# Kernel tuning notes

Hardware: AMD Instinct MI355X
Metric: run time of the kernel (lower is better)

## Reference

```python
import jax, jax.numpy as jnp
import numpy as np

B, T, D_IN = 64, 365, 10
D_MODEL, N_HEAD, D_K = 256, 16, 8
D_HEAD = D_MODEL // N_HEAD  # 16, value head dim
MAX_POS = 365 + 2 * 30      # max_position + 2*max_temporal_shift = 425
BN_EPS = 1e-5


def _pos_table(n_pos, d, temp=1000.0):
    # standard sinusoidal table (frozen in the original via Embedding.from_pretrained)
    pos = np.arange(n_pos)[:, None].astype(np.float64)
    i = np.arange(d)[None, :]
    angle = pos / np.power(temp, 2 * (i // 2) / d)
    tab = np.where(i % 2 == 0, np.sin(angle), np.cos(angle))
    return jnp.asarray(tab, jnp.float32)

POS_TABLE = _pos_table(MAX_POS, D_MODEL)


def _linear_layer(x, W, b, g, beta):
    # LinearLayer = Linear -> BatchNorm1d (train-mode batch stats, per-feature) -> ReLU
    y = x @ W.T + b
    ax = tuple(range(y.ndim - 1))
    mu = y.mean(ax, keepdims=True)
    var = y.var(ax, keepdims=True)  # biased var, matches torch BN
    y = (y - mu) * jax.lax.rsqrt(var + BN_EPS) * g + beta
    return jax.nn.relu(y)


def _forward(positions, x, w1, b1, g1, e1, w2, b2, g2, e2, w3, b3, g3, e3,
             ws1, ws2, wi, bi, gi, ei, wk, bk, wq, bq, wm, bm, gm, em,
             wd1, bd1, gd1, ed1, wd2, bd2, gd2, ed2, wc, bc):
    # channel MLP encoder: 10 -> 64 -> 128 -> 256
    out = _linear_layer(x, w1, b1, g1, e1)
    out = _linear_layer(out, w2, b2, g2, e2)
    out = _linear_layer(out, w3, b3, g3, e3)                    # [B,T,256]
    # channel SE attention: avgpool over time, 2 linears (no bias), sigmoid, residual
    pooled = out.mean(axis=1, keepdims=True)                     # [B,1,256]
    att = jax.nn.sigmoid(jax.nn.relu(pooled @ ws1.T) @ ws2.T)    # [B,1,256]
    out = att * pooled + out                                     # broadcast residual
    # temporal attention block
    h = _linear_layer(out, wi, bi, gi, ei)                       # inconv -> [B,T,256]
    e = h + POS_TABLE[positions]                                 # add positional encoding
    q = (e @ wq.T + bq).reshape(B, T, N_HEAD, D_K)
    k = (e @ wk.T + bk).reshape(B, T, N_HEAD, D_K)
    v = e.reshape(B, T, N_HEAD, D_HEAD)
    # 'cross' attention: full score matrix, mean over key dim, softmax over query dim
    scores = jnp.einsum('bthd,bshd->bhts', q, k) / jnp.sqrt(jnp.float32(D_K))  # [B,H,T,T]
    scores = scores.mean(axis=-1)                                # [B,H,T]
    a = jax.nn.softmax(scores, axis=-1)                          # [B,H,T]
    y = jnp.einsum('bht,bthe->bhe', a, v).reshape(B, D_MODEL)    # [B,256]
    y = _linear_layer(y, wm, bm, gm, em)                         # mlp 256 -> 128
    # decoder: 128 -> 64 -> 32 -> num_classes
    z = _linear_layer(y, wd1, bd1, gd1, ed1)
    z = _linear_layer(z, wd2, bd2, gd2, ed2)
    return z @ wc.T + bc                                         # logits [B,10]


def setup_inputs():
    key = jax.random.key(0)
    ks = jax.random.split(key, 16)
    n = lambda i, sh: jax.random.normal(ks[i], sh, jnp.float32) * 0.05
    z, o = jnp.zeros, jnp.ones
    return {
        'x': jax.random.normal(ks[0], (B, T, D_IN), jnp.float32),
        'positions': jnp.sort(jax.random.randint(ks[1], (B, T), 0, MAX_POS), axis=-1),
        'w1': n(2, (64, D_IN)), 'b1': z(64), 'g1': o(64), 'e1': z(64),
        'w2': n(3, (128, 64)), 'b2': z(128), 'g2': o(128), 'e2': z(128),
        'w3': n(4, (256, 128)), 'b3': z(256), 'g3': o(256), 'e3': z(256),
        'ws1': n(5, (16, 256)), 'ws2': n(6, (256, 16)),
        'wi': n(7, (256, 256)), 'bi': z(256), 'gi': o(256), 'ei': z(256),
        'wk': n(8, (128, 256)), 'bk': z(128),
        'wq': n(9, (128, 256)), 'bq': z(128),
        'wm': n(10, (128, 256)), 'bm': z(128), 'gm': o(128), 'em': z(128),
        'wd1': n(11, (64, 128)), 'bd1': z(64), 'gd1': o(64), 'ed1': z(64),
        'wd2': n(12, (32, 64)), 'bd2': z(32), 'gd2': o(32), 'ed2': z(32),
        'wc': n(13, (10, 32)), 'bc': z(10),
    }


def reference(x, positions, w1, b1, g1, e1, w2, b2, g2, e2, w3, b3, g3, e3,
              ws1, ws2, wi, bi, gi, ei, wk, bk, wq, bq, wm, bm, gm, em,
              wd1, bd1, gd1, ed1, wd2, bd2, gd2, ed2, wc, bc):
    return _forward(positions, x, w1, b1, g1, e1, w2, b2, g2, e2, w3, b3, g3, e3,
                    ws1, ws2, wi, bi, gi, ei, wk, bk, wq, bq, wm, bm, gm, em,
                    wd1, bd1, gd1, ed1, wd2, bd2, gd2, ed2, wc, bc)
```

## Files before the change

### kernel.cpp

```cpp
#include <hip/hip_runtime.h>
#include <hip/hip_bf16.h>
#include <math.h>

#define TT 365
#define BT 23360
#define NPOS 425

typedef __hip_bfloat16 bf16;
typedef __attribute__((ext_vector_type(8))) short s16x8;
typedef __attribute__((ext_vector_type(4))) float f32x4;

__device__ __forceinline__ float b2f(bf16 v) { return __bfloat162float(v); }
__device__ __forceinline__ bf16  f2b(float v) { return __float2bfloat16(v); }
__device__ __forceinline__ float u2f(unsigned u) { return __uint_as_float(u); }
__device__ __forceinline__ short f2bs(float v) { bf16 h = __float2bfloat16(v); return *reinterpret_cast<short*>(&h); }
__device__ __forceinline__ void unpack8(uint4 raw, float* v) {
    v[0] = u2f(raw.x << 16); v[1] = u2f(raw.x & 0xffff0000u);
    v[2] = u2f(raw.y << 16); v[3] = u2f(raw.y & 0xffff0000u);
    v[4] = u2f(raw.z << 16); v[5] = u2f(raw.z & 0xffff0000u);
    v[6] = u2f(raw.w << 16); v[7] = u2f(raw.w & 0xffff0000u);
}

__global__ __launch_bounds__(256) void prep_kernel(
    float* __restrict__ stats, float* __restrict__ pooled, float* __restrict__ esum,
    const float* __restrict__ w2, const float* __restrict__ w3, const float* __restrict__ wi,
    const float* __restrict__ wq,
    bf16* __restrict__ whi, bf16* __restrict__ wlo, float* __restrict__ tab)
{
    int i = blockIdx.x * 256 + threadIdx.x;
    if (i < 2048)  { stats[i] = 0.f; return; }  i -= 2048;
    if (i < 16384) { pooled[i] = 0.f; return; } i -= 16384;
    if (i < 16384) { esum[i] = 0.f; return; }   i -= 16384;
    if (i < 139264) {
        float w;
        if      (i < 8192)   w = w2[i];
        else if (i < 40960)  w = w3[i - 8192];
        else if (i < 106496) w = wi[i - 40960];
        else                 w = wq[i - 106496];
        bf16 h = f2b(w);
        whi[i] = h;
        wlo[i] = f2b(w - b2f(h));
        return;
    } i -= 139264;
    if (i < 108800) {
        int c = i & 255, p = i >> 8;
        float e = (float)(2 * (c >> 1)) * (1.f / 256.f);
        float ang = (float)p * exp2f(-e * 9.96578428466209f);
        tab[i] = (c & 1) ? cosf(ang) : sinf(ang);
    }
}

__global__ __launch_bounds__(256) void gemm_l1_kernel(
    const float* __restrict__ x,
    const float* __restrict__ W, const float* __restrict__ bias,
    bf16* __restrict__ Y, float* __restrict__ stats)
{
    const int t  = threadIdx.x;
    const int tx = t & 15, ty = t >> 4;
    const int row0 = blockIdx.x * 64;
    __shared__ float As[64][17];
    __shared__ float Ws[16][65];
    __shared__ float red_s[4][64];
    __shared__ float red_q[4][64];
    float acc[4][4];
#pragma unroll
    for (int rr = 0; rr < 4; ++rr)
#pragma unroll
        for (int cc = 0; cc < 4; ++cc) acc[rr][cc] = 0.f;
#pragma unroll
    for (int i = 0; i < 4; ++i) {
        int idx = t + i * 256, r = idx >> 4, c = idx & 15;
        As[r][c] = (c < 10) ? x[(size_t)(row0 + r) * 10 + c] : 0.f;
    }
#pragma unroll
    for (int i = 0; i < 4; ++i) {
        int idx = t + i * 256, c = idx >> 4, kk = idx & 15;
        Ws[kk][c] = (kk < 10) ? W[(size_t)c * 10 + kk] : 0.f;
    }
    __syncthreads();
#pragma unroll
    for (int kk = 0; kk < 10; ++kk) {
        float a[4];
#pragma unroll
        for (int rr = 0; rr < 4; ++rr) a[rr] = As[ty * 4 + rr][kk];
#pragma unroll
        for (int cc = 0; cc < 4; ++cc) {
            float w = Ws[kk][cc * 16 + tx];
#pragma unroll
            for (int rr = 0; rr < 4; ++rr) acc[rr][cc] = fmaf(a[rr], w, acc[rr][cc]);
        }
    }
    float s_cc[4], q_cc[4];
#pragma unroll
    for (int cc = 0; cc < 4; ++cc) { s_cc[cc] = 0.f; q_cc[cc] = 0.f; }
#pragma unroll
    for (int rr = 0; rr < 4; ++rr) {
        int row = row0 + ty * 4 + rr;
#pragma unroll
        for (int cc = 0; cc < 4; ++cc) {
            int col = cc * 16 + tx;
            float v = acc[rr][cc] + bias[col];
            Y[(size_t)row * 64 + col] = f2b(v);
            s_cc[cc] += v; q_cc[cc] += v * v;
        }
    }
    int w = t >> 6;
#pragma unroll
    for (int cc = 0; cc < 4; ++cc) {
        float s = s_cc[cc], q = q_cc[cc];
        s += __shfl_xor(s, 16); q += __shfl_xor(q, 16);
        s += __shfl_xor(s, 32); q += __shfl_xor(q, 32);
        if ((t & 63) < 16) { red_s[w][cc * 16 + tx] = s; red_q[w][cc * 16 + tx] = q; }
    }
    __syncthreads();
    if (t < 64) {
        float s = red_s[0][t] + red_s[1][t] + red_s[2][t] + red_s[3][t];
        float q = red_q[0][t] + red_q[1][t] + red_q[2][t] + red_q[3][t];
        atomicAdd(&stats[t], s);
        atomicAdd(&stats[256 + t], q);
    }
}

template<int MODE, int K>
__global__ __launch_bounds__(256) void mfma_gemm(
    const bf16* __restrict__ A,
    const bf16* __restrict__ Whi, const bf16* __restrict__ Wlo,
    const float* __restrict__ bias,
    bf16* __restrict__ Y, int ldY, float* __restrict__ stats,
    const float* __restrict__ bnstats, const float* __restrict__ bng,
    const float* __restrict__ bnb, const float* __restrict__ sebuf)
{
    constexpr int KC = (K > 128) ? 128 : K;
    __shared__ s16x8 Wl[2][KC / 8][64];
    __shared__ float red_s[4][64];
    __shared__ float red_q[4][64];
    __shared__ float scb[MODE ? K : 1];
    __shared__ float shb[MODE ? K : 1];
    const int t = threadIdx.x, wave = t >> 6, lane = t & 63;
    const int n16 = lane & 15, quad = lane >> 4;
    const int m0 = blockIdx.x * 64 + wave * 16;
    const int col0 = blockIdx.y * 64;
    const int sc_ = t & 63, skg0 = t >> 6;
    const bf16* gh = Whi + (size_t)(col0 + sc_) * K;
    const bf16* gl = Wlo + (size_t)(col0 + sc_) * K;
#pragma unroll
    for (int kg = skg0; kg < KC / 8; kg += 4) {
        Wl[0][kg][sc_] = *(const s16x8*)(gh + kg * 8);
        Wl[1][kg][sc_] = *(const s16x8*)(gl + kg * 8);
    }
    if (MODE) {
        if (t < K) {
            float mu = bnstats[t] * (1.f / (float)BT);
            float var = bnstats[256 + t] * (1.f / (float)BT) - mu * mu;
            float sc = rsqrtf(var + 1e-5f) * bng[t];
            scb[t] = sc; shb[t] = bnb[t] - mu * sc;
        }
    }
    __syncthreads();
    const int arow = m0 + n16;
    const float* sev = (MODE == 2) ? (sebuf + (arow / TT) * 256) : nullptr;
    const bf16* Ap = A + (size_t)arow * K + quad * 8;
    s16x8 af[K / 32];
#pragma unroll
    for (int i = 0; i < K / 32; ++i) {
        s16x8 raw = *(const s16x8*)(Ap + i * 32);
        if (MODE) {
            int kb = i * 32 + quad * 8;
#pragma unroll
            for (int j = 0; j < 8; ++j) {
                float y = u2f(((unsigned)(unsigned short)raw[j]) << 16);
                float v = fmaxf(fmaf(y, scb[kb + j], shb[kb + j]), 0.f);
                if (MODE == 2) v += sev[kb + j];
                raw[j] = f2bs(v);
            }
        }
        af[i] = raw;
    }
    f32x4 acc[4];
    f32x4 zero = {0.f, 0.f, 0.f, 0.f};
#pragma unroll
    for (int ct = 0; ct < 4; ++ct) acc[ct] = zero;
#pragma unroll
    for (int kc = 0; kc < K; kc += KC) {
        if (kc) {
            __syncthreads();
#pragma unroll
            for (int kg = skg0; kg < KC / 8; kg += 4) {
                Wl[0][kg][sc_] = *(const s16x8*)(gh + kc + kg * 8);
                Wl[1][kg][sc_] = *(const s16x8*)(gl + kc + kg * 8);
            }
            __syncthreads();
        }
#pragma unroll
        for (int i = 0; i < KC / 32; ++i) {
            const int kgq = i * 4 + quad;
            const s16x8 a = af[(kc >> 5) + i];
#pragma unroll
            for (int ct = 0; ct < 4; ++ct) {
                s16x8 bl = Wl[1][kgq][ct * 16 + n16];
                s16x8 bh = Wl[0][kgq][ct * 16 + n16];
                acc[ct] = __builtin_amdgcn_mfma_f32_16x16x32_bf16(a, bl, acc[ct], 0, 0, 0);
                acc[ct] = __builtin_amdgcn_mfma_f32_16x16x32_bf16(a, bh, acc[ct], 0, 0, 0);
            }
        }
    }
#pragma unroll
    for (int ct = 0; ct < 4; ++ct) {
        int col = col0 + ct * 16 + n16;
        float bv = bias[col];
        float s = 0.f, q = 0.f;
#pragma unroll
        for (int r = 0; r < 4; ++r) {
            float v = acc[ct][r] + bv;
            int row = m0 + quad * 4 + r;
            Y[(size_t)row * ldY + col] = f2b(v);
            s += v; q += v * v;
        }
        s += __shfl_xor(s, 16); q += __shfl_xor(q, 16);
        s += __shfl_xor(s, 32); q += __shfl_xor(q, 32);
        if (quad == 0) { red_s[wave][ct * 16 + n16] = s; red_q[wave][ct * 16 + n16] = q; }
    }
    if (stats) {
        __syncthreads();
        if (t < 64) {
            float s = red_s[0][t] + red_s[1][t] + red_s[2][t] + red_s[3][t];
            float q = red_q[0][t] + red_q[1][t] + red_q[2][t] + red_q[3][t];
            atomicAdd(&stats[col0 + t], s);
            atomicAdd(&stats[256 + col0 + t], q);
        }
    }
}

__global__ __launch_bounds__(256) void pool_partial_kernel(
    const bf16* __restrict__ Y3, const float* __restrict__ stats,
    const float* __restrict__ g3, const float* __restrict__ e3,
    float* __restrict__ pooled)
{
    const int b = blockIdx.x, part = blockIdx.y, t = threadIdx.x;
    const int cg = t & 31, rs = t >> 5;
    __shared__ float scb[256], shb[256];
    __shared__ float pp[8][256];
    {
        float mu = stats[t] * (1.f / (float)BT);
        float var = stats[256 + t] * (1.f / (float)BT) - mu * mu;
        float sc = rsqrtf(var + 1e-5f) * g3[t];
        scb[t] = sc; shb[t] = e3[t] - mu * sc;
    }
    __syncthreads();
    float acc[8] = {0.f,0.f,0.f,0.f,0.f,0.f,0.f,0.f};
    const int r0 = part * 46;
#pragma unroll
    for (int i = 0; i < 6; ++i) {
        int l = rs + i * 8;
        int r = r0 + l;
        if (l < 46 && r < TT) {
            uint4 raw = *(const uint4*)(Y3 + ((size_t)b * TT + r) * 256 + cg * 8);
            float v[8];
            unpack8(raw, v);
#pragma unroll
            for (int j = 0; j < 8; ++j)
                acc[j] += fmaxf(fmaf(v[j], scb[cg * 8 + j], shb[cg * 8 + j]), 0.f);
        }
    }
#pragma unroll
    for (int j = 0; j < 8; ++j) pp[rs][cg * 8 + j] = acc[j];
    __syncthreads();
    float s = 0.f;
#pragma unroll
    for (int r = 0; r < 8; ++r) s += pp[r][t];
    atomicAdd(&pooled[b * 256 + t], s);
}

__global__ __launch_bounds__(256) void esum_kernel(const bf16* __restrict__ e,
                                                   float* __restrict__ esum)
{
    const int b = blockIdx.x, part = blockIdx.y, t = threadIdx.x;
    const int cg = t & 31, rs = t >> 5;
    __shared__ float pp[8][256];
    float acc[8] = {0.f,0.f,0.f,0.f,0.f,0.f,0.f,0.f};
    const int r0 = part * 46;
#pragma unroll
    for (int i = 0; i < 6; ++i) {
        int l = rs + i * 8;
        int r = r0 + l;
        if (l < 46 && r < TT) {
            uint4 raw = *(const uint4*)(e + ((size_t)b * TT + r) * 256 + cg * 8);
            float v[8];
            unpack8(raw, v);
#pragma unroll
            for (int j = 0; j < 8; ++j) acc[j] += v[j];
        }
    }
#pragma unroll
    for (int j = 0; j < 8; ++j) pp[rs][cg * 8 + j] = acc[j];
    __syncthreads();
    float s = 0.f;
#pragma unroll
    for (int r = 0; r < 8; ++r) s += pp[r][t];
    atomicAdd(&esum[b * 256 + t], s);
}

__global__ __launch_bounds__(256) void se_mlp_kernel(const float* __restrict__ pooled,
                                                     const float* __restrict__ ws1,
                                                     const float* __restrict__ ws2,
                                                     float* __restrict__ se) {
    int b = blockIdx.x, f = threadIdx.x;
    __shared__ float pl[256];
    __shared__ float hidden[16];
    float p = pooled[b * 256 + f] * (1.f / (float)TT);
    pl[f] = p;
    __syncthreads();
    if (f < 16) {
        float h = 0.f;
        for (int k2 = 0; k2 < 256; ++k2) h = fmaf(pl[k2], ws1[f * 256 + k2], h);
        hidden[f] = fmaxf(h, 0.f);
    }
    __syncthreads();
    float a = 0.f;
    for (int k2 = 0; k2 < 16; ++k2) a = fmaf(hidden[k2], ws2[f * 16 + k2], a);
    a = 1.f / (1.f + expf(-a));
    se[b * 256 + f] = a * p;
}

__global__ __launch_bounds__(256) void bnrelu8_kernel(
    const bf16* __restrict__ Y, const float* __restrict__ stats,
    const float* __restrict__ g, const float* __restrict__ beta,
    bf16* __restrict__ Out, const float* __restrict__ tab, const int* __restrict__ pos) {
    int i = (blockIdx.x * 256 + threadIdx.x) * 8;
    int col = i & 255, row = i >> 8;
    uint4 raw = *(const uint4*)(Y + i);
    float v[8];
    unpack8(raw, v);
    const float invM = 1.f / (float)BT;
    const float* tr = tab + pos[row] * 256 + col;
    bf16 tmp[8] __attribute__((aligned(16)));
#pragma unroll
    for (int j = 0; j < 8; ++j) {
        float mu  = stats[col + j] * invM;
        float var = stats[256 + col + j] * invM - mu * mu;
        float o = (v[j] - mu) * rsqrtf(var + 1e-5f) * g[col + j] + beta[col + j];
        tmp[j] = f2b(fmaxf(o, 0.f) + tr[j]);
    }
    *(uint4*)(Out + i) = *(const uint4*)tmp;
}

__global__ __launch_bounds__(64) void attn_kernel(
    const bf16* __restrict__ q, const bf16* __restrict__ e,
    const float* __restrict__ esum, const float* __restrict__ wk,
    const float* __restrict__ bk, float* __restrict__ yv)
{
    __shared__ float aw[368];
    const int b = blockIdx.x, h = blockIdx.y;
    const int lane = threadIdx.x;
    float4 es = *(const float4*)(esum + b * 256 + lane * 4);
    float ks[8];
#pragma unroll
    for (int d = 0; d < 8; ++d) {
        float4 wv = *(const float4*)(wk + (size_t)(h * 8 + d) * 256 + lane * 4);
        ks[d] = es.x * wv.x + es.y * wv.y + es.z * wv.z + es.w * wv.w;
    }
#pragma unroll
    for (int off = 1; off < 64; off <<= 1)
#pragma unroll
        for (int d = 0; d < 8; ++d) ks[d] += __shfl_xor(ks[d], off);
#pragma unroll
    for (int d = 0; d < 8; ++d) ks[d] += (float)TT * bk[h * 8 + d];
    const float scale = 1.f / (sqrtf(8.f) * (float)TT);
    const bf16* qb = q + (size_t)b * TT * 128 + h * 8;
    float sv[6];
    float m = -1e30f;
#pragma unroll
    for (int i = 0; i < 6; ++i) {
        int r = lane + i * 64;
        float s = -1e30f;
        if (r < TT) {
            uint4 raw = *(const uint4*)(qb + (size_t)r * 128);
            float v[8];
            unpack8(raw, v);
            float dot = 0.f;
#pragma unroll
            for (int j = 0; j < 8; ++j) dot = fmaf(v[j], ks[j], dot);
            s = dot * scale;
        }
        sv[i] = s;
        m = fmaxf(m, s);
    }
#pragma unroll
    for (int off = 1; off < 64; off <<= 1) m = fmaxf(m, __shfl_xor(m, off));
    float sum = 0.f;
#pragma unroll
    for (int i = 0; i < 6; ++i) {
        float ev = (sv[i] > -1e29f) ? expf(sv[i] - m) : 0.f;
        sv[i] = ev; sum += ev;
    }
#pragma unroll
    for (int off = 1; off < 64; off <<= 1) sum += __shfl_xor(sum, off);
    float inv = 1.f / sum;
#pragma unroll
    for (int i = 0; i < 6; ++i) {
        int r = lane + i * 64;
        if (r < TT) aw[r] = sv[i] * inv;
    }
    __syncthreads();
    const int half = lane & 1, rs = lane >> 1;
    float acc[8] = {0.f,0.f,0.f,0.f,0.f,0.f,0.f,0.f};
    const bf16* ebase = e + (size_t)b * TT * 256 + h * 16 + half * 8;
#pragma unroll
    for (int i = 0; i < 12; ++i) {
        int r = rs + i * 32;
        if (r < TT) {
            uint4 raw = *(const uint4*)(ebase + (size_t)r * 256);
            float v[8];
            unpack8(raw, v);
            float a = aw[r];
#pragma unroll
            for (int j = 0; j < 8; ++j) acc[j] = fmaf(a, v[j], acc[j]);
        }
    }
#pragma unroll
    for (int off = 2; off < 64; off <<= 1)
#pragma unroll
        for (int j = 0; j < 8; ++j) acc[j] += __shfl_xor(acc[j], off);
    if (lane < 2) {
        float* op = yv + b * 256 + h * 16 + half * 8;
#pragma unroll
        for (int j = 0; j < 8; ++j) op[j] = acc[j];
    }
}

__global__ __launch_bounds__(1024) void tail_kernel(
    const float* __restrict__ yv,
    const float* wm, const float* bm, const float* gm, const float* em,
    const float* wd1, const float* bd1, const float* gd1, const float* ed1,
    const float* wd2, const float* bd2, const float* gd2, const float* ed2,
    const float* wc, const float* bc, float* __restrict__ out)
{
    __shared__ float lds[12352];
    const int t = threadIdx.x;
    const int r = t & 63, cg = t >> 6;
    float* Xq  = lds;
    float* Wp  = lds + 4160;
    float* Z1t = lds;
    float* Wd1h = lds + 8192;
    float* Z2t = lds;
    float* Wd2 = lds + 4096;
    float* Z3t = lds + 6144;
    float* WcL = lds + 8192;

    float acc1[8] = {0.f,0.f,0.f,0.f,0.f,0.f,0.f,0.f};
    const int c01 = cg * 8;
    for (int p = 0; p < 4; ++p) {
        __syncthreads();
        for (int i = t; i < 4096; i += 1024) {
            int kk = i & 63, rr = i >> 6;
            Xq[kk * 65 + rr] = yv[rr * 256 + p * 64 + kk];
        }
        {
            const float4* wm4 = (const float4*)wm;
            float4* Wp4 = (float4*)Wp;
            for (int i = t; i < 2048; i += 1024) {
                int kk4 = i & 15, c = i >> 4;
                Wp4[c * 16 + kk4] = wm4[c * 64 + p * 16 + kk4];
            }
        }
        __syncthreads();
#pragma unroll 4
        for (int k4 = 0; k4 < 16; ++k4) {
            float xv[4];
#pragma unroll
            for (int j = 0; j < 4; ++j) xv[j] = Xq[(k4 * 4 + j) * 65 + r];
#pragma unroll
            for (int c = 0; c < 8; ++c) {
                float4 w = *(const float4*)(Wp + (c01 + c) * 64 + k4 * 4);
                acc1[c] = fmaf(xv[0], w.x, acc1[c]);
                acc1[c] = fmaf(xv[1], w.y, acc1[c]);
                acc1[c] = fmaf(xv[2], w.z, acc1[c]);
                acc1[c] = fmaf(xv[3], w.w, acc1[c]);
            }
        }
    }
    float z1v[8];
#pragma unroll
    for (int c = 0; c < 8; ++c) {
        float v = acc1[c] + bm[c01 + c];
        float s = v, q = v * v;
#pragma unroll
        for (int off = 1; off < 64; off <<= 1) { s += __shfl_xor(s, off); q += __shfl_xor(q, off); }
        float mu = s * (1.f / 64.f), var = q * (1.f / 64.f) - mu * mu;
        z1v[c] = fmaxf((v - mu) * rsqrtf(var + 1e-5f) * gm[c01 + c] + em[c01 + c], 0.f);
    }
    __syncthreads();
#pragma unroll
    for (int c = 0; c < 8; ++c) Z1t[(c01 + c) * 64 + r] = z1v[c];
    float acc2[4] = {0.f, 0.f, 0.f, 0.f};
    const int c02 = cg * 4;
    for (int ph = 0; ph < 2; ++ph) {
        __syncthreads();
        {
            const float4* s4 = (const float4*)wd1;
            float4* d4 = (float4*)Wd1h;
            int kk4 = t & 15, c = t >> 4;
            d4[c * 16 + kk4] = s4[c * 32 + ph * 16 + kk4];
        }
        __syncthreads();
#pragma unroll 4
        for (int k4 = 0; k4 < 16; ++k4) {
            float xv[4];
#pragma unroll
            for (int j = 0; j < 4; ++j) xv[j] = Z1t[(ph * 64 + k4 * 4 + j) * 64 + r];
#pragma unroll
            for (int c = 0; c < 4; ++c) {
                float4 w = *(const float4*)(Wd1h + (c02 + c) * 64 + k4 * 4);
                acc2[c] = fmaf(xv[0], w.x, acc2[c]);
                acc2[c] = fmaf(xv[1], w.y, acc2[c]);
                acc2[c] = fmaf(xv[2], w.z, acc2[c]);
                acc2[c] = fmaf(xv[3], w.w, acc2[c]);
            }
        }
    }
    float z2v[4];
#pragma unroll
    for (int c = 0; c < 4; ++c) {
        float v = acc2[c] + bd1[c02 + c];
        float s = v, q = v * v;
#pragma unroll
        for (int off = 1; off < 64; off <<= 1) { s += __shfl_xor(s, off); q += __shfl_xor(q, off); }
        float mu = s * (1.f / 64.f), var = q * (1.f / 64.f) - mu * mu;
        z2v[c] = fmaxf((v - mu) * rsqrtf(var + 1e-5f) * gd1[c02 + c] + ed1[c02 + c], 0.f);
    }
    __syncthreads();
#pragma unroll
    for (int c = 0; c < 4; ++c) Z2t[(c02 + c) * 64 + r] = z2v[c];
    {
        const float4* s4 = (const float4*)wd2;
        float4* d4 = (float4*)Wd2;
        if (t < 512) d4[t] = s4[t];
    }
    __syncthreads();
    float acc3[2] = {0.f, 0.f};
    const int c03 = cg * 2;
#pragma unroll 4
    for (int k4 = 0; k4 < 16; ++k4) {
        float xv[4];
#pragma unroll
        for (int j = 0; j < 4; ++j) xv[j] = Z2t[(k4 * 4 + j) * 64 + r];
#pragma unroll
        for (int c = 0; c < 2; ++c) {
            float4 w = *(const float4*)(Wd2 + (c03 + c) * 64 + k4 * 4);
            acc3[c] = fmaf(xv[0], w.x, acc3[c]);
            acc3[c] = fmaf(xv[1], w.y, acc3[c]);
            acc3[c] = fmaf(xv[2], w.z, acc3[c]);
            acc3[c] = fmaf(xv[3], w.w, acc3[c]);
        }
    }
#pragma unroll
    for (int c = 0; c < 2; ++c) {
        float v = acc3[c] + bd2[c03 + c];
        float s = v, q = v * v;
#pragma unroll
        for (int off = 1; off < 64; off <<= 1) { s += __shfl_xor(s, off); q += __shfl_xor(q, off); }
        float mu = s * (1.f / 64.f), var = q * (1.f / 64.f) - mu * mu;
        Z3t[(c03 + c) * 64 + r] = fmaxf((v - mu) * rsqrtf(var + 1e-5f) * gd2[c03 + c] + ed2[c03 + c], 0.f);
    }
    if (t < 80) ((float4*)WcL)[t] = ((const float4*)wc)[t];
    __syncthreads();
    if (t < 640) {
        int rr = t / 10, c = t % 10;
        float s = bc[c];
#pragma unroll
        for (int kk = 0; kk < 32; ++kk) s = fmaf(Z3t[kk * 64 + rr], WcL[c * 32 + kk], s);
        out[t] = s;
    }
}


extern "C" void kernel_launch(void* const* d_in, const int* in_sizes, int n_in,
                              void* d_out, int out_size, void* d_ws, size_t ws_size,
                              hipStream_t stream) {
    (void)in_sizes; (void)n_in; (void)out_size; (void)ws_size;
    const float* x  = (const float*)d_in[0];
    const int* pos  = (const int*)d_in[1];
    const float *w1 = (const float*)d_in[2],  *b1 = (const float*)d_in[3],
                *g1 = (const float*)d_in[4],  *e1 = (const float*)d_in[5];
    const float *w2 = (const float*)d_in[6],  *b2 = (const float*)d_in[7],
                *g2 = (const float*)d_in[8],  *e2 = (const float*)d_in[9];
    const float *w3 = (const float*)d_in[10], *b3 = (const float*)d_in[11],
                *g3 = (const float*)d_in[12], *e3 = (const float*)d_in[13];
    const float *ws1 = (const float*)d_in[14], *ws2 = (const float*)d_in[15];
    const float *wi = (const float*)d_in[16], *bi = (const float*)d_in[17],
                *gi = (const float*)d_in[18], *ei = (const float*)d_in[19];
    const float *wk = (const float*)d_in[20], *bk = (const float*)d_in[21];
    const float *wq = (const float*)d_in[22], *bq = (const float*)d_in[23];
    const float *wm = (const float*)d_in[24], *bm = (const float*)d_in[25],
                *gm = (const float*)d_in[26], *em = (const float*)d_in[27];
    const float *wd1 = (const float*)d_in[28], *bd1 = (const float*)d_in[29],
                *gd1 = (const float*)d_in[30], *ed1 = (const float*)d_in[31];
    const float *wd2 = (const float*)d_in[32], *bd2 = (const float*)d_in[33],
                *gd2 = (const float*)d_in[34], *ed2 = (const float*)d_in[35];
    const float *wc = (const float*)d_in[36], *bc = (const float*)d_in[37];
    float* out = (float*)d_out;

    char* w8 = (char*)d_ws;
    bf16*  actA   = (bf16*)(w8);
    bf16*  actB   = (bf16*)(w8 + 11960320);
    bf16*  whi    = (bf16*)(w8 + 23920640);
    bf16*  wlo    = (bf16*)(w8 + 24199168);
    float* tab    = (float*)(w8 + 24477696);
    float* stats  = (float*)(w8 + 24912896);
    float* pooled = (float*)(w8 + 24921088);
    float* sebuf  = (float*)(w8 + 24986624);
    float* esum   = (float*)(w8 + 25052160);
    float* yvb    = (float*)(w8 + 25117696);

    prep_kernel<<<1105, 256, 0, stream>>>(stats, pooled, esum, w2, w3, wi, wq, whi, wlo, tab);
    gemm_l1_kernel<<<365, 256, 0, stream>>>(x, w1, b1, actB, stats);
    mfma_gemm<1, 64><<<dim3(365, 2), 256, 0, stream>>>(actB, whi, wlo, b2,
                                                       actA, 128, stats + 512, stats, g1, e1, nullptr);
    mfma_gemm<1, 128><<<dim3(365, 4), 256, 0, stream>>>(actA, whi + 8192, wlo + 8192, b3,
                                                        actB, 256, stats + 1024, stats + 512, g2, e2, nullptr);
    pool_partial_kernel<<<dim3(64, 8), 256, 0, stream>>>(actB, stats + 1024, g3, e3, pooled);
    se_mlp_kernel<<<64, 256, 0, stream>>>(pooled, ws1, ws2, sebuf);
    mfma_gemm<2, 256><<<dim3(365, 4), 256, 0, stream>>>(actB, whi + 40960, wlo + 40960, bi,
                                                        actA, 256, stats + 1536, stats + 1024, g3, e3, sebuf);
    bnrelu8_kernel<<<BT * 256 / 2048, 256, 0, stream>>>(actA, stats + 1536, gi, ei, actB, tab, pos);
    esum_kernel<<<dim3(64, 8), 256, 0, stream>>>(actB, esum);
    mfma_gemm<0, 256><<<dim3(365, 2), 256, 0, stream>>>(actB, whi + 106496, wlo + 106496, bq,
                                                        actA, 128, nullptr, nullptr, nullptr, nullptr, nullptr);
    attn_kernel<<<dim3(64, 16), 64, 0, stream>>>(actA, actB, esum, wk, bk, yvb);
    tail_kernel<<<1, 1024, 0, stream>>>(yvb, wm, bm, gm, em, wd1, bd1, gd1, ed1,
                                        wd2, bd2, gd2, ed2, wc, bc, out);
}
```

Before: 324.7 us.

## Restructure tail MLP kernel with swizzled LDS rows and direct weight loads

Rewrites the tail kernel that runs the three post-attention Linear+BN+ReLU layers and the classifier. It stages the whole yv matrix once into LDS using an XOR-swizzled row-major layout and reads weights straight from global memory with wave-uniform (readfirstlane) indices, instead of re-staging transposed tiles and weights in four phases. BatchNorm stats are now computed by a few threads scanning columns in LDS rather than by wave shuffles, and the linear biases are dropped because batch-norm mean subtraction cancels them. This removes barriers and redundant LDS staging, at the cost of serial column-stat loops and more LDS.

```diff
diff --git a/kernel.cpp b/kernel.cpp
--- a/kernel.cpp
+++ b/kernel.cpp
@@ -9,6 +9,7 @@
 typedef __hip_bfloat16 bf16;
 typedef __attribute__((ext_vector_type(8))) short s16x8;
 typedef __attribute__((ext_vector_type(4))) float f32x4;
+typedef __attribute__((ext_vector_type(2))) float f32x2;
 
 __device__ __forceinline__ float b2f(bf16 v) { return __bfloat162float(v); }
 __device__ __forceinline__ bf16  f2b(float v) { return __float2bfloat16(v); }
@@ -430,145 +431,194 @@
 
 __global__ __launch_bounds__(1024) void tail_kernel(
     const float* __restrict__ yv,
-    const float* wm, const float* bm, const float* gm, const float* em,
-    const float* wd1, const float* bd1, const float* gd1, const float* ed1,
-    const float* wd2, const float* bd2, const float* gd2, const float* ed2,
-    const float* wc, const float* bc, float* __restrict__ out)
+    const float* __restrict__ wm, const float* __restrict__ bm,
+    const float* __restrict__ gm, const float* __restrict__ em,
+    const float* __restrict__ wd1, const float* __restrict__ bd1,
+    const float* __restrict__ gd1, const float* __restrict__ ed1,
+    const float* __restrict__ wd2, const float* __restrict__ bd2,
+    const float* __restrict__ gd2, const float* __restrict__ ed2,
+    const float* __restrict__ wc, const float* __restrict__ bc,
+    float* __restrict__ out)
 {
-    __shared__ float lds[12352];
+    (void)bm; (void)bd1; (void)bd2;
+    __shared__ float lds[16384];
     const int t = threadIdx.x;
-    const int r = t & 63, cg = t >> 6;
-    float* Xq  = lds;
-    float* Wp  = lds + 4160;
-    float* Z1t = lds;
-    float* Wd1h = lds + 8192;
-    float* Z2t = lds;
-    float* Wd2 = lds + 4096;
-    float* Z3t = lds + 6144;
-    float* WcL = lds + 8192;
-
+    const int r = t & 63;
+    const int rx = r & 7;
+    const int cgu = __builtin_amdgcn_readfirstlane(t >> 6);
+
+#pragma unroll
+    for (int p = 0; p < 4; ++p) {
+        int idx = p * 1024 + t;
+        int row = idx >> 6, c4 = idx & 63;
+        float4 v = *(const float4*)(yv + (size_t)idx * 4);
+        *(float4*)&lds[(row * 64 + (c4 ^ (row & 7))) * 4] = v;
+    }
+    __syncthreads();
+
+    const int c01 = cgu * 8;
     float acc1[8] = {0.f,0.f,0.f,0.f,0.f,0.f,0.f,0.f};
-    const int c01 = cg * 8;
-    for (int p = 0; p < 4; ++p) {
-        __syncthreads();
-        for (int i = t; i < 4096; i += 1024) {
-            int kk = i & 63, rr = i >> 6;
-            Xq[kk * 65 + rr] = yv[rr * 256 + p * 64 + kk];
-        }
-        {
-            const float4* wm4 = (const float4*)wm;
-            float4* Wp4 = (float4*)Wp;
-            for (int i = t; i < 2048; i += 1024) {
-                int kk4 = i & 15, c = i >> 4;
-                Wp4[c * 16 + kk4] = wm4[c * 64 + p * 16 + kk4];
+    {
+        const float4* w4 = (const float4*)wm;
+#pragma unroll 4
+        for (int k4 = 0; k4 < 64; ++k4) {
+            float4 xv = *(const float4*)&lds[(r * 64 + (k4 ^ rx)) * 4];
+#pragma unroll
+            for (int c = 0; c < 8; ++c) {
+                float4 w = w4[(c01 + c) * 64 + k4];
+                acc1[c] = fmaf(xv.x, w.x, acc1[c]);
+                acc1[c] = fmaf(xv.y, w.y, acc1[c]);
+                acc1[c] = fmaf(xv.z, w.z, acc1[c]);
+                acc1[c] = fmaf(xv.w, w.w, acc1[c]);
             }
         }
-        __syncthreads();
+    }
+    __syncthreads();
+#pragma unroll
+    for (int j = 0; j < 2; ++j) {
+        int c4 = cgu * 2 + j;
+        float4 v = { acc1[j*4+0], acc1[j*4+1], acc1[j*4+2], acc1[j*4+3] };
+        *(float4*)&lds[(r * 32 + (c4 ^ rx)) * 4] = v;
+    }
+    __syncthreads();
+    if (t < 128) {
+        float s = 0.f, q = 0.f;
+        int c4 = t >> 2, cr = t & 3;
+        for (int row = 0; row < 64; ++row) {
+            float v = lds[(row * 32 + (c4 ^ (row & 7))) * 4 + cr];
+            s += v; q += v * v;
+        }
+        float mu = s * (1.f/64.f), var = q * (1.f/64.f) - mu * mu;
+        float sc = rsqrtf(var + 1e-5f) * gm[t];
+        lds[8192 + t] = sc;
+        lds[8320 + t] = em[t] - mu * sc;
+    }
+    __syncthreads();
+#pragma unroll
+    for (int j = 0; j < 2; ++j) {
+        int c4 = cgu * 2 + j;
+        float4 sc = *(const float4*)&lds[8192 + c4 * 4];
+        float4 sh = *(const float4*)&lds[8320 + c4 * 4];
+        float* p = &lds[(r * 32 + (c4 ^ rx)) * 4];
+        float4 v = *(const float4*)p;
+        v.x = fmaxf(fmaf(v.x, sc.x, sh.x), 0.f);
+        v.y = fmaxf(fmaf(v.y, sc.y, sh.y), 0.f);
+        v.z = fmaxf(fmaf(v.z, sc.z, sh.z), 0.f);
+        v.w = fmaxf(fmaf(v.w, sc.w, sh.w), 0.f);
+        *(float4*)p = v;
+    }
+    __syncthreads();
+
+    const int c02 = cgu * 4;
+    float acc2[4] = {0.f,0.f,0.f,0.f};
+    {
+        const float4* w4 = (const float4*)wd1;
+#pragma unroll 4
+        for (int k4 = 0; k4 < 32; ++k4) {
+            float4 xv = *(const float4*)&lds[(r * 32 + (k4 ^ rx)) * 4];
+#pragma unroll
+            for (int c = 0; c < 4; ++c) {
+                float4 w = w4[(c02 + c) * 32 + k4];
+                acc2[c] = fmaf(xv.x, w.x, acc2[c]);
+                acc2[c] = fmaf(xv.y, w.y, acc2[c]);
+                acc2[c] = fmaf(xv.z, w.z, acc2[c]);
+                acc2[c] = fmaf(xv.w, w.w, acc2[c]);
+            }
+        }
+    }
+    {
+        float4 v = { acc2[0], acc2[1], acc2[2], acc2[3] };
+        *(float4*)&lds[8448 + (r * 16 + (cgu ^ rx)) * 4] = v;
+    }
+    __syncthreads();
+    if (t < 64) {
+        float s = 0.f, q = 0.f;
+        int c4 = t >> 2, cr = t & 3;
+        for (int row = 0; row < 64; ++row) {
+            float v = lds[8448 + (row * 16 + (c4 ^ (row & 7))) * 4 + cr];
+            s += v; q += v * v;
+        }
+        float mu = s * (1.f/64.f), var = q * (1.f/64.f) - mu * mu;
+        float sc = rsqrtf(var + 1e-5f) * gd1[t];
+        lds[12544 + t] = sc;
+        lds[12608 + t] = ed1[t] - mu * sc;
+    }
+    __syncthreads();
+    {
+        int c4 = cgu;
+        float4 sc = *(const float4*)&lds[12544 + c4 * 4];
+        float4 sh = *(const float4*)&lds[12608 + c4 * 4];
+        float* p = &lds[8448 + (r * 16 + (c4 ^ rx)) * 4];
+        float4 v = *(const float4*)p;
+        v.x = fmaxf(fmaf(v.x, sc.x, sh.x), 0.f);
+        v.y = fmaxf(fmaf(v.y, sc.y, sh.y), 0.f);
+        v.z = fmaxf(fmaf(v.z, sc.z, sh.z), 0.f);
+        v.w = fmaxf(fmaf(v.w, sc.w, sh.w), 0.f);
+        *(float4*)p = v;
+    }
+    __syncthreads();
+
+    const int c03 = cgu * 2;
+    float acc3[2] = {0.f, 0.f};
+    {
+        const float4* w4 = (const float4*)wd2;
 #pragma unroll 4
         for (int k4 = 0; k4 < 16; ++k4) {
-            float xv[4];
-#pragma unroll
-            for (int j = 0; j < 4; ++j) xv[j] = Xq[(k4 * 4 + j) * 65 + r];
-#pragma unroll
-            for (int c = 0; c < 8; ++c) {
-                float4 w = *(const float4*)(Wp + (c01 + c) * 64 + k4 * 4);
-                acc1[c] = fmaf(xv[0], w.x, acc1[c]);
-                acc1[c] = fmaf(xv[1], w.y, acc1[c]);
-                acc1[c] = fmaf(xv[2], w.z, acc1[c]);
-                acc1[c] = fmaf(xv[3], w.w, acc1[c]);
+            float4 xv = *(const float4*)&lds[8448 + (r * 16 + (k4 ^ rx)) * 4];
+#pragma unroll
+            for (int c = 0; c < 2; ++c) {
+                float4 w = w4[(c03 + c) * 16 + k4];
+                acc3[c] = fmaf(xv.x, w.x, acc3[c]);
+                acc3[c] = fmaf(xv.y, w.y, acc3[c]);
+                acc3[c] = fmaf(xv.z, w.z, acc3[c]);
+                acc3[c] = fmaf(xv.w, w.w, acc3[c]);
             }
         }
     }
-    float z1v[8];
-#pragma unroll
-    for (int c = 0; c < 8; ++c) {
-        float v = acc1[c] + bm[c01 + c];
-        float s = v, q = v * v;
-#pragma unroll
-        for (int off = 1; off < 64; off <<= 1) { s += __shfl_xor(s, off); q += __shfl_xor(q, off); }
-        float mu = s * (1.f / 64.f), var = q * (1.f / 64.f) - mu * mu;
-        z1v[c] = fmaxf((v - mu) * rsqrtf(var + 1e-5f) * gm[c01 + c] + em[c01 + c], 0.f);
-    }
-    __syncthreads();
-#pragma unroll
-    for (int c = 0; c < 8; ++c) Z1t[(c01 + c) * 64 + r] = z1v[c];
-    float acc2[4] = {0.f, 0.f, 0.f, 0.f};
-    const int c02 = cg * 4;
-    for (int ph = 0; ph < 2; ++ph) {
-        __syncthreads();
-        {
-            const float4* s4 = (const float4*)wd1;
-            float4* d4 = (float4*)Wd1h;
-            int kk4 = t & 15, c = t >> 4;
-            d4[c * 16 + kk4] = s4[c * 32 + ph * 16 + kk4];
-        }
-        __syncthreads();
-#pragma unroll 4
-        for (int k4 = 0; k4 < 16; ++k4) {
-            float xv[4];
-#pragma unroll
-            for (int j = 0; j < 4; ++j) xv[j] = Z1t[(ph * 64 + k4 * 4 + j) * 64 + r];
-#pragma unroll
-            for (int c = 0; c < 4; ++c) {
-                float4 w = *(const float4*)(Wd1h + (c02 + c) * 64 + k4 * 4);
-                acc2[c] = fmaf(xv[0], w.x, acc2[c]);
-                acc2[c] = fmaf(xv[1], w.y, acc2[c]);
-                acc2[c] = fmaf(xv[2], w.z, acc2[c]);
-                acc2[c] = fmaf(xv[3], w.w, acc2[c]);
-            }
-        }
-    }
-    float z2v[4];
-#pragma unroll
-    for (int c = 0; c < 4; ++c) {
-        float v = acc2[c] + bd1[c02 + c];
-        float s = v, q = v * v;
-#pragma unroll
-        for (int off = 1; off < 64; off <<= 1) { s += __shfl_xor(s, off); q += __shfl_xor(q, off); }
-        float mu = s * (1.f / 64.f), var = q * (1.f / 64.f) - mu * mu;
-        z2v[c] = fmaxf((v - mu) * rsqrtf(var + 1e-5f) * gd1[c02 + c] + ed1[c02 + c], 0.f);
-    }
-    __syncthreads();
-#pragma unroll
-    for (int c = 0; c < 4; ++c) Z2t[(c02 + c) * 64 + r] = z2v[c];
     {
-        const float4* s4 = (const float4*)wd2;
-        float4* d4 = (float4*)Wd2;
-        if (t < 512) d4[t] = s4[t];
-    }
-    __syncthreads();
-    float acc3[2] = {0.f, 0.f};
-    const int c03 = cg * 2;
-#pragma unroll 4
-    for (int k4 = 0; k4 < 16; ++k4) {
-        float xv[4];
-#pragma unroll
-        for (int j = 0; j < 4; ++j) xv[j] = Z2t[(k4 * 4 + j) * 64 + r];
-#pragma unroll
-        for (int c = 0; c < 2; ++c) {
-            float4 w = *(const float4*)(Wd2 + (c03 + c) * 64 + k4 * 4);
-            acc3[c] = fmaf(xv[0], w.x, acc3[c]);
-            acc3[c] = fmaf(xv[1], w.y, acc3[c]);
-            acc3[c] = fmaf(xv[2], w.z, acc3[c]);
-            acc3[c] = fmaf(xv[3], w.w, acc3[c]);
-        }
-    }
-#pragma unroll
-    for (int c = 0; c < 2; ++c) {
-        float v = acc3[c] + bd2[c03 + c];
-        float s = v, q = v * v;
-#pragma unroll
-        for (int off = 1; off < 64; off <<= 1) { s += __shfl_xor(s, off); q += __shfl_xor(q, off); }
-        float mu = s * (1.f / 64.f), var = q * (1.f / 64.f) - mu * mu;
-        Z3t[(c03 + c) * 64 + r] = fmaxf((v - mu) * rsqrtf(var + 1e-5f) * gd2[c03 + c] + ed2[c03 + c], 0.f);
-    }
-    if (t < 80) ((float4*)WcL)[t] = ((const float4*)wc)[t];
+        f32x2 v = { acc3[0], acc3[1] };
+        *(f32x2*)&lds[12672 + (r * 8 + ((cgu >> 1) ^ rx)) * 4 + (cgu & 1) * 2] = v;
+    }
+    __syncthreads();
+    if (t < 32) {
+        float s = 0.f, q = 0.f;
+        int c4 = t >> 2, cr = t & 3;
+        for (int row = 0; row < 64; ++row) {
+            float v = lds[12672 + (row * 8 + (c4 ^ (row & 7))) * 4 + cr];
+            s += v; q += v * v;
+        }
+        float mu = s * (1.f/64.f), var = q * (1.f/64.f) - mu * mu;
+        float sc = rsqrtf(var + 1e-5f) * gd2[t];
+        lds[14720 + t] = sc;
+        lds[14752 + t] = ed2[t] - mu * sc;
+    }
+    __syncthreads();
+    if (t < 512) {
+        int rr = t & 63, c4 = t >> 6;
+        float4 sc = *(const float4*)&lds[14720 + c4 * 4];
+        float4 sh = *(const float4*)&lds[14752 + c4 * 4];
+        float* p = &lds[12672 + (rr * 8 + (c4 ^ (rr & 7))) * 4];
+        float4 v = *(const float4*)p;
+        v.x = fmaxf(fmaf(v.x, sc.x, sh.x), 0.f);
+        v.y = fmaxf(fmaf(v.y, sc.y, sh.y), 0.f);
+        v.z = fmaxf(fmaf(v.z, sc.z, sh.z), 0.f);
+        v.w = fmaxf(fmaf(v.w, sc.w, sh.w), 0.f);
+        *(float4*)p = v;
+    }
     __syncthreads();
     if (t < 640) {
-        int rr = t / 10, c = t % 10;
+        int rr = t / 10, c = t - rr * 10;
+        const float4* wc4 = (const float4*)wc;
         float s = bc[c];
 #pragma unroll
-        for (int kk = 0; kk < 32; ++kk) s = fmaf(Z3t[kk * 64 + rr], WcL[c * 32 + kk], s);
+        for (int k4 = 0; k4 < 8; ++k4) {
+            float4 xv = *(const float4*)&lds[12672 + (rr * 8 + (k4 ^ (rr & 7))) * 4];
+            float4 w = wc4[c * 8 + k4];
+            s = fmaf(xv.x, w.x, s);
+            s = fmaf(xv.y, w.y, s);
+            s = fmaf(xv.z, w.z, s);
+            s = fmaf(xv.w, w.w, s);
+        }
         out[t] = s;
     }
 }
```

Result: no change. 319.6 us (-1.6%).

## Split single-block tail MLP into three multi-block kernels and drop BN-cancelled biases

Applied to the files above, without the earlier changes.

Replaces the single 1024-thread tail kernel with three kernels: the 256->128 layer over 16 blocks, the 128->64 layer over 8 blocks, and the final 64->32->10 layers in one block. Weights are read directly from global memory instead of being staged in LDS. Linear biases that batch norm cancels are dropped. The goal is to spread the tail across more compute units, at the cost of two extra launches and global round-trips for the intermediates, which reuse the esum and sebuf workspace.

```diff
diff --git a/kernel.cpp b/kernel.cpp
--- a/kernel.cpp
+++ b/kernel.cpp
@@ -428,40 +428,22 @@
     }
 }
 
-__global__ __launch_bounds__(1024) void tail_kernel(
-    const float* __restrict__ yv,
-    const float* wm, const float* bm, const float* gm, const float* em,
-    const float* wd1, const float* bd1, const float* gd1, const float* ed1,
-    const float* wd2, const float* bd2, const float* gd2, const float* ed2,
-    const float* wc, const float* bc, float* __restrict__ out)
-{
-    __shared__ float lds[12352];
-    const int t = threadIdx.x;
-    const int r = t & 63, cg = t >> 6;
-    float* Xq  = lds;
-    float* Wp  = lds + 4160;
-    float* Z1t = lds;
-    float* Wd1h = lds + 8192;
-    float* Z2t = lds;
-    float* Wd2 = lds + 4096;
-    float* Z3t = lds + 6144;
-    float* WcL = lds + 8192;
-
-    float acc1[8] = {0.f,0.f,0.f,0.f,0.f,0.f,0.f,0.f};
-    const int c01 = cg * 8;
+
+__global__ __launch_bounds__(256) void tail_m_kernel(
+    const float* __restrict__ yv, const float* __restrict__ wm,
+    const float* __restrict__ gm, const float* __restrict__ em,
+    float* __restrict__ z1)
+{
+    __shared__ float Xq[4160];
+    const int t = threadIdx.x, r = t & 63, cw = t >> 6;
+    const int c0 = blockIdx.x * 8 + cw * 2;
+    const float4* wf4 = (const float4*)wm;
+    float acc[2] = {0.f, 0.f};
     for (int p = 0; p < 4; ++p) {
-        __syncthreads();
-        for (int i = t; i < 4096; i += 1024) {
+        if (p) __syncthreads();
+        for (int i = t; i < 4096; i += 256) {
             int kk = i & 63, rr = i >> 6;
             Xq[kk * 65 + rr] = yv[rr * 256 + p * 64 + kk];
-        }
-        {
-            const float4* wm4 = (const float4*)wm;
-            float4* Wp4 = (float4*)Wp;
-            for (int i = t; i < 2048; i += 1024) {
-                int kk4 = i & 15, c = i >> 4;
-                Wp4[c * 16 + kk4] = wm4[c * 64 + p * 16 + kk4];
-            }
         }
         __syncthreads();
 #pragma unroll 4
@@ -470,106 +452,125 @@
 #pragma unroll
             for (int j = 0; j < 4; ++j) xv[j] = Xq[(k4 * 4 + j) * 65 + r];
 #pragma unroll
-            for (int c = 0; c < 8; ++c) {
-                float4 w = *(const float4*)(Wp + (c01 + c) * 64 + k4 * 4);
-                acc1[c] = fmaf(xv[0], w.x, acc1[c]);
-                acc1[c] = fmaf(xv[1], w.y, acc1[c]);
-                acc1[c] = fmaf(xv[2], w.z, acc1[c]);
-                acc1[c] = fmaf(xv[3], w.w, acc1[c]);
+            for (int c = 0; c < 2; ++c) {
+                float4 w = wf4[(c0 + c) * 64 + p * 16 + k4];
+                acc[c] = fmaf(xv[0], w.x, acc[c]);
+                acc[c] = fmaf(xv[1], w.y, acc[c]);
+                acc[c] = fmaf(xv[2], w.z, acc[c]);
+                acc[c] = fmaf(xv[3], w.w, acc[c]);
             }
         }
     }
-    float z1v[8];
-#pragma unroll
-    for (int c = 0; c < 8; ++c) {
-        float v = acc1[c] + bm[c01 + c];
+#pragma unroll
+    for (int c = 0; c < 2; ++c) {
+        float v = acc[c];
         float s = v, q = v * v;
 #pragma unroll
         for (int off = 1; off < 64; off <<= 1) { s += __shfl_xor(s, off); q += __shfl_xor(q, off); }
         float mu = s * (1.f / 64.f), var = q * (1.f / 64.f) - mu * mu;
-        z1v[c] = fmaxf((v - mu) * rsqrtf(var + 1e-5f) * gm[c01 + c] + em[c01 + c], 0.f);
-    }
-    __syncthreads();
-#pragma unroll
-    for (int c = 0; c < 8; ++c) Z1t[(c01 + c) * 64 + r] = z1v[c];
-    float acc2[4] = {0.f, 0.f, 0.f, 0.f};
-    const int c02 = cg * 4;
-    for (int ph = 0; ph < 2; ++ph) {
-        __syncthreads();
-        {
-            const float4* s4 = (const float4*)wd1;
-            float4* d4 = (float4*)Wd1h;
-            int kk4 = t & 15, c = t >> 4;
-            d4[c * 16 + kk4] = s4[c * 32 + ph * 16 + kk4];
+        float sc = rsqrtf(var + 1e-5f) * gm[c0 + c], sh = em[c0 + c] - mu * sc;
+        z1[r * 128 + c0 + c] = fmaxf(fmaf(v, sc, sh), 0.f);
+    }
+}
+
+__global__ __launch_bounds__(256) void tail_d1_kernel(
+    const float* __restrict__ z1, const float* __restrict__ wd1,
+    const float* __restrict__ gd1, const float* __restrict__ ed1,
+    float* __restrict__ z2)
+{
+    __shared__ float Xq[4160];
+    const int t = threadIdx.x, r = t & 63, cw = t >> 6;
+    const int c0 = blockIdx.x * 8 + cw * 2;
+    const float4* wf4 = (const float4*)wd1;
+    float acc[2] = {0.f, 0.f};
+    for (int p = 0; p < 2; ++p) {
+        if (p) __syncthreads();
+        for (int i = t; i < 4096; i += 256) {
+            int kk = i & 63, rr = i >> 6;
+            Xq[kk * 65 + rr] = z1[rr * 128 + p * 64 + kk];
         }
         __syncthreads();
 #pragma unroll 4
         for (int k4 = 0; k4 < 16; ++k4) {
             float xv[4];
 #pragma unroll
-            for (int j = 0; j < 4; ++j) xv[j] = Z1t[(ph * 64 + k4 * 4 + j) * 64 + r];
-#pragma unroll
-            for (int c = 0; c < 4; ++c) {
-                float4 w = *(const float4*)(Wd1h + (c02 + c) * 64 + k4 * 4);
-                acc2[c] = fmaf(xv[0], w.x, acc2[c]);
-                acc2[c] = fmaf(xv[1], w.y, acc2[c]);
-                acc2[c] = fmaf(xv[2], w.z, acc2[c]);
-                acc2[c] = fmaf(xv[3], w.w, acc2[c]);
+            for (int j = 0; j < 4; ++j) xv[j] = Xq[(k4 * 4 + j) * 65 + r];
+#pragma unroll
+            for (int c = 0; c < 2; ++c) {
+                float4 w = wf4[(c0 + c) * 32 + p * 16 + k4];
+                acc[c] = fmaf(xv[0], w.x, acc[c]);
+                acc[c] = fmaf(xv[1], w.y, acc[c]);
+                acc[c] = fmaf(xv[2], w.z, acc[c]);
+                acc[c] = fmaf(xv[3], w.w, acc[c]);
             }
         }
     }
-    float z2v[4];
-#pragma unroll
-    for (int c = 0; c < 4; ++c) {
-        float v = acc2[c] + bd1[c02 + c];
+#pragma unroll
+    for (int c = 0; c < 2; ++c) {
+        float v = acc[c];
         float s = v, q = v * v;
 #pragma unroll
         for (int off = 1; off < 64; off <<= 1) { s += __shfl_xor(s, off); q += __shfl_xor(q, off); }
         float mu = s * (1.f / 64.f), var = q * (1.f / 64.f) - mu * mu;
-        z2v[c] = fmaxf((v - mu) * rsqrtf(var + 1e-5f) * gd1[c02 + c] + ed1[c02 + c], 0.f);
-    }
-    __syncthreads();
-#pragma unroll
-    for (int c = 0; c < 4; ++c) Z2t[(c02 + c) * 64 + r] = z2v[c];
-    {
-        const float4* s4 = (const float4*)wd2;
-        float4* d4 = (float4*)Wd2;
-        if (t < 512) d4[t] = s4[t];
-    }
-    __syncthreads();
-    float acc3[2] = {0.f, 0.f};
-    const int c03 = cg * 2;
+        float sc = rsqrtf(var + 1e-5f) * gd1[c0 + c], sh = ed1[c0 + c] - mu * sc;
+        z2[r * 64 + c0 + c] = fmaxf(fmaf(v, sc, sh), 0.f);
+    }
+}
+
+__global__ __launch_bounds__(256) void tail_d2c_kernel(
+    const float* __restrict__ z2, const float* __restrict__ wd2,
+    const float* __restrict__ gd2, const float* __restrict__ ed2,
+    const float* __restrict__ wc, const float* __restrict__ bc,
+    float* __restrict__ out)
+{
+    __shared__ float Xq[4160];
+    __shared__ float Z3t[2048];
+    __shared__ float WcL[320];
+    const int t = threadIdx.x, r = t & 63, cw = t >> 6;
+    const int c03 = cw * 8;
+    for (int i = t; i < 4096; i += 256) {
+        int kk = i & 63, rr = i >> 6;
+        Xq[kk * 65 + rr] = z2[rr * 64 + kk];
+    }
+    if (t < 80) ((float4*)WcL)[t] = ((const float4*)wc)[t];
+    __syncthreads();
+    const float4* wf4 = (const float4*)wd2;
+    float acc[8] = {0.f,0.f,0.f,0.f,0.f,0.f,0.f,0.f};
 #pragma unroll 4
     for (int k4 = 0; k4 < 16; ++k4) {
         float xv[4];
 #pragma unroll
-        for (int j = 0; j < 4; ++j) xv[j] = Z2t[(k4 * 4 + j) * 64 + r];
-#pragma unroll
-        for (int c = 0; c < 2; ++c) {
-            float4 w = *(const float4*)(Wd2 + (c03 + c) * 64 + k4 * 4);
-            acc3[c] = fmaf(xv[0], w.x, acc3[c]);
-            acc3[c] = fmaf(xv[1], w.y, acc3[c]);
-            acc3[c] = fmaf(xv[2], w.z, acc3[c]);
-            acc3[c] = fmaf(xv[3], w.w, acc3[c]);
-        }
-    }
-#pragma unroll
-    for (int c = 0; c < 2; ++c) {
-        float v = acc3[c] + bd2[c03 + c];
+        for (int j = 0; j < 4; ++j) xv[j] = Xq[(k4 * 4 + j) * 65 + r];
+#pragma unroll
+        for (int c = 0; c < 8; ++c) {
+            float4 w = wf4[(c03 + c) * 16 + k4];
+            acc[c] = fmaf(xv[0], w.x, acc[c]);
+            acc[c] = fmaf(xv[1], w.y, acc[c]);
+            acc[c] = fmaf(xv[2], w.z, acc[c]);
+            acc[c] = fmaf(xv[3], w.w, acc[c]);
+        }
+    }
+#pragma unroll
+    for (int c = 0; c < 8; ++c) {
+        float v = acc[c];
         float s = v, q = v * v;
 #pragma unroll
         for (int off = 1; off < 64; off <<= 1) { s += __shfl_xor(s, off); q += __shfl_xor(q, off); }
         float mu = s * (1.f / 64.f), var = q * (1.f / 64.f) - mu * mu;
-        Z3t[(c03 + c) * 64 + r] = fmaxf((v - mu) * rsqrtf(var + 1e-5f) * gd2[c03 + c] + ed2[c03 + c], 0.f);
-    }
-    if (t < 80) ((float4*)WcL)[t] = ((const float4*)wc)[t];
-    __syncthreads();
-    if (t < 640) {
-        int rr = t / 10, c = t % 10;
-        float s = bc[c];
-#pragma unroll
-        for (int kk = 0; kk < 32; ++kk) s = fmaf(Z3t[kk * 64 + rr], WcL[c * 32 + kk], s);
-        out[t] = s;
+        float sc = rsqrtf(var + 1e-5f) * gd2[c03 + c], sh = ed2[c03 + c] - mu * sc;
+        Z3t[(c03 + c) * 64 + r] = fmaxf(fmaf(v, sc, sh), 0.f);
+    }
+    __syncthreads();
+#pragma unroll
+    for (int i = 0; i < 3; ++i) {
+        int idx = t + i * 256;
+        if (idx < 640) {
+            int rr = idx / 10, c = idx - rr * 10;
+            float s = bc[c];
+#pragma unroll
+            for (int kk = 0; kk < 32; ++kk) s = fmaf(Z3t[kk * 64 + rr], WcL[c * 32 + kk], s);
+            out[idx] = s;
+        }
     }
 }
 
@@ -599,6 +600,7 @@
                 *gd2 = (const float*)d_in[34], *ed2 = (const float*)d_in[35];
     const float *wc = (const float*)d_in[36], *bc = (const float*)d_in[37];
     float* out = (float*)d_out;
+    (void)bm; (void)bd1; (void)bd2;
 
     char* w8 = (char*)d_ws;
     bf16*  actA   = (bf16*)(w8);
@@ -611,6 +613,8 @@
     float* sebuf  = (float*)(w8 + 24986624);
     float* esum   = (float*)(w8 + 25052160);
     float* yvb    = (float*)(w8 + 25117696);
+    float* z1     = esum;
+    float* z2     = sebuf;
 
     prep_kernel<<<1105, 256, 0, stream>>>(stats, pooled, esum, w2, w3, wi, wq, whi, wlo, tab);
     gemm_l1_kernel<<<365, 256, 0, stream>>>(x, w1, b1, actB, stats);
@@ -627,6 +631,7 @@
     mfma_gemm<0, 256><<<dim3(365, 2), 256, 0, stream>>>(actB, whi + 106496, wlo + 106496, bq,
                                                         actA, 128, nullptr, nullptr, nullptr, nullptr, nullptr);
     attn_kernel<<<dim3(64, 16), 64, 0, stream>>>(actA, actB, esum, wk, bk, yvb);
-    tail_kernel<<<1, 1024, 0, stream>>>(yvb, wm, bm, gm, em, wd1, bd1, gd1, ed1,
-                                        wd2, bd2, gd2, ed2, wc, bc, out);
-}
+    tail_m_kernel<<<16, 256, 0, stream>>>(yvb, wm, gm, em, z1);
+    tail_d1_kernel<<<8, 256, 0, stream>>>(z1, wd1, gd1, ed1, z2);
+    tail_d2c_kernel<<<1, 256, 0, stream>>>(z2, wd2, gd2, ed2, wc, bc, out);
+}
```

Result: faster. 316.0 us (-2.7%).
